# Performance work log

Measured on AMD Instinct MI355X. Metric: run time of the kernel, lower is better.

Reference implementation:

```python
import jax, jax.numpy as jnp
import numpy as np

N = 500000      # nodes
F_IN = 10       # node_features
HID = 32        # DCRNN hidden
OUT = 2         # out_features
E = 8000000     # edges (unused in math since K=1, kept for interface fidelity)


def setup_inputs() -> dict:
    key = jax.random.key(0)
    ks = jax.random.split(key, 12)
    d_in = F_IN + HID  # 42: DConv input is cat([X, H])
    s = 0.1
    return {
        "x": jax.random.normal(ks[0], (N, F_IN), dtype=jnp.float32),
        "edge_index": jax.random.randint(ks[1], (2, E), 0, N, dtype=jnp.int64),
        "edge_weight": jax.random.uniform(ks[2], (E,), dtype=jnp.float32),
        "h": jax.random.normal(ks[3], (N, HID), dtype=jnp.float32),
        # DConv weights: torch shape (2, K=1, in, out); K dim squeezed -> (2, in, out)
        "W_z": jax.random.normal(ks[4], (2, d_in, HID), dtype=jnp.float32) * s,
        "b_z": jnp.zeros((HID,), dtype=jnp.float32),
        "W_r": jax.random.normal(ks[5], (2, d_in, HID), dtype=jnp.float32) * s,
        "b_r": jnp.zeros((HID,), dtype=jnp.float32),
        "W_h": jax.random.normal(ks[6], (2, d_in, HID), dtype=jnp.float32) * s,
        "b_h": jnp.zeros((HID,), dtype=jnp.float32),
        "W_lin": jax.random.normal(ks[7], (OUT, HID), dtype=jnp.float32) * s,
        "b_lin": jnp.zeros((OUT,), dtype=jnp.float32),
    }


def _dconv_k1(xh, W, b):
    # K=1 DConv: out/in diffusion weights collapse to a single dense transform
    return xh @ (W[0] + W[1]) + b


def reference(x, edge_index, edge_weight, h, W_z, b_z, W_r, b_r, W_h, b_h, W_lin, b_lin):
    # DCRNN GRU step (edge_index/edge_weight unused because K=1)
    xh = jnp.concatenate([x, h], axis=1)                  # [N, F_IN+HID]
    z = jax.nn.sigmoid(_dconv_k1(xh, W_z, b_z))           # update gate
    r = jax.nn.sigmoid(_dconv_k1(xh, W_r, b_r))           # reset gate
    xrh = jnp.concatenate([x, r * h], axis=1)
    h_tilde = jnp.tanh(_dconv_k1(xrh, W_h, b_h))
    h_new = z * h + (1.0 - z) * h_tilde                   # [N, HID]
    out = jnp.maximum(h_new, 0.0) @ W_lin.T + b_lin       # ReLU + Linear head, [N, OUT]
    return (out, h_new)
```

## Files before the change

### kernel.cpp

```cpp
#include <hip/hip_runtime.h>
#include <stdint.h>

static constexpr int N_NODES = 500000;
static constexpr int STR     = 56;

typedef __attribute__((ext_vector_type(8))) short short8;
typedef __attribute__((ext_vector_type(4))) float f32x4;


__device__ __forceinline__ float bfdec(uint32_t b){
  union{uint32_t u; float f;} c; c.u = b << 16; return c.f;
}
__device__ __forceinline__ uint32_t bfrne(float f){
  union{float f; uint32_t u;} c; c.f = f;
  return (c.u + 0x7fffu + ((c.u >> 16) & 1u)) >> 16;
}
__device__ __forceinline__ uint32_t pack2(float a, float b){
  return bfrne(a) | (bfrne(b) << 16);
}
__device__ __forceinline__ float sigmoid_fast(float x){
  float e = __expf(-x);
  return __builtin_amdgcn_rcpf(1.0f + e);
}
__device__ __forceinline__ float tanh_fast(float x){
  float e = __expf(2.0f * x);
  return 1.0f - 2.0f * __builtin_amdgcn_rcpf(e + 1.0f);
}

__device__ bool detect_f32_words(const uint32_t* w, int K){
  float m = 0.0f;
  for (int i = 0; i < K; i++) m = fmaxf(m, fabsf(bfdec(w[i] & 0xffffu)));
  return !(m < 1e6f);
}
__device__ __forceinline__ float wload(const void* p, int idx, bool f32w){
  if (f32w) return ((const float*)p)[idx];
  return bfdec(((const uint16_t*)p)[idx]);
}

__global__ void prep_kernel(const void* __restrict__ Wz,
                            const void* __restrict__ bz,
                            const void* __restrict__ Wr,
                            const void* __restrict__ br,
                            const void* __restrict__ Wh,
                            const void* __restrict__ bh,
                            const void* __restrict__ Wl,
                            const void* __restrict__ bl,
                            const uint32_t* __restrict__ xg,
                            const uint32_t* __restrict__ hg,
                            float* __restrict__ ws)
{
  const bool f32w = detect_f32_words((const uint32_t*)Wz, 64);
  uint16_t* wsh = (uint16_t*)ws;
  float*    wsf = ws;
  int i = blockIdx.x * 256 + threadIdx.x;
  if (i < 5376) {
    float v = 0.0f;
    if (i < 3584) {
      int col = i / STR, k = i - col * STR;
      if (k < 42) {
        const void* Wp = (col < 32) ? Wz : Wr;
        int j = (col < 32) ? col : col - 32;
        int src = k * 32 + j;
        v = wload(Wp, src, f32w) + wload(Wp, 1344 + src, f32w);
      }
    } else {
      int t2 = i - 3584;
      int col = t2 / STR, k = t2 - col * STR;
      if (k < 42) {
        int src = k * 32 + col;
        v = wload(Wh, src, f32w) + wload(Wh, 1344 + src, f32w);
      }
    }
    wsh[i] = (uint16_t)bfrne(v);
  } else if (i < 5440) {
    int r = i - 5376;
    wsh[i] = (uint16_t)bfrne(wload(Wl, r, f32w));
  } else if (i < 5538) {
    int r = i - 5440;
    if      (r < 32) wsf[2720 + r]      = wload(bz, r,     f32w);
    else if (r < 64) wsf[2752 + (r-32)] = wload(br, r-32,  f32w);
    else if (r < 96) wsf[2784 + (r-64)] = wload(bh, r-64,  f32w);
    else             wsf[2816 + (r-96)] = wload(bl, r-96,  f32w);
  } else if (i == 5568) {
    wsf[2818] = detect_f32_words(xg, 256) ? 1.0f : 0.0f;
  } else if (i == 5569) {
    wsf[2819] = detect_f32_words(hg, 256) ? 1.0f : 0.0f;
  }
}

__global__ __launch_bounds__(256, 4) void dcrnn_kernel(
    const uint32_t* __restrict__ xg,
    const uint32_t* __restrict__ hg,
    const float*    __restrict__ ws,
    float* __restrict__ out0,
    float* __restrict__ outh)
{
  __shared__ __align__(16) uint16_t w_u16[96 * STR];
  __shared__ __align__(16) uint16_t xh_u16[256 * STR];

  const int t  = threadIdx.x;
  const int nd = blockIdx.x * 256 + t;
  const bool valid = nd < N_NODES;
  const float* wsf = ws;
  const bool x_f32 = wsf[2818] != 0.0f;
  const bool h_f32 = wsf[2819] != 0.0f;

  const uint4* wsq = (const uint4*)ws;
  for (int i = t; i < 672; i += 256) ((uint4*)w_u16)[i] = wsq[i];

  uint32_t rw[24];
  #pragma unroll
  for (int i = 0; i < 24; i++) rw[i] = 0u;
  if (valid) {
    if (x_f32) {
      const float2* xr = (const float2*)((const float*)xg + (size_t)nd * 10);
      #pragma unroll
      for (int i = 0; i < 5; i++){ float2 v = xr[i]; rw[i] = pack2(v.x, v.y); }
    } else {
      const uint32_t* xr = xg + (size_t)nd * 5;
      #pragma unroll
      for (int i = 0; i < 5; i++) rw[i] = xr[i];
    }
    if (h_f32) {
      const float4* hr = (const float4*)((const float*)hg + (size_t)nd * 32);
      #pragma unroll
      for (int i = 0; i < 8; i++){
        float4 v = hr[i];
        rw[5 + 2*i]     = pack2(v.x, v.y);
        rw[5 + 2*i + 1] = pack2(v.z, v.w);
      }
    } else {
      const uint4* hr = (const uint4*)(hg + (size_t)nd * 16);
      #pragma unroll
      for (int i = 0; i < 4; i++){
        uint4 v = hr[i];
        rw[5 + 4*i]     = v.x; rw[5 + 4*i + 1] = v.y;
        rw[5 + 4*i + 2] = v.z; rw[5 + 4*i + 3] = v.w;
      }
    }
  }
  {
    uint4* dst = (uint4*)(xh_u16 + t * STR);
    #pragma unroll
    for (int c = 0; c < 6; c++)
      dst[c] = make_uint4(rw[4*c], rw[4*c+1], rw[4*c+2], rw[4*c+3]);
  }
  __syncthreads();

  const int l = t & 63, w = t >> 6;
  const int lo16 = l & 15, g = l >> 4;
  uint16_t* xwm = xh_u16 + (w * 64) * STR;

  const float bzc0 = wsf[2720 + lo16], bzc1 = wsf[2736 + lo16];
  const float brc0 = wsf[2752 + lo16], brc1 = wsf[2768 + lo16];
  const float bhc0 = wsf[2784 + lo16], bhc1 = wsf[2800 + lo16];
  const float blc  = (lo16 < 2) ? wsf[2816 + lo16] : 0.0f;

  const short8 zero8 = {0,0,0,0,0,0,0,0};

  short8 bzr_lo[4], bzr_hi[4];
  #pragma unroll
  for (int nt = 0; nt < 4; nt++){
    const uint16_t* brow = w_u16 + (nt*16 + lo16) * STR;
    bzr_lo[nt] = *(const short8*)(brow + g*8);
    bzr_hi[nt] = zero8;
    if (g < 2) bzr_hi[nt] = *(const short8*)(brow + 32 + g*8);
  }
  short8 bh_lo[2], bh_hi[2];
  #pragma unroll
  for (int nt = 0; nt < 2; nt++){
    const uint16_t* brow = w_u16 + 3584 + (nt*16 + lo16) * STR;
    bh_lo[nt] = *(const short8*)(brow + g*8);
    bh_hi[nt] = zero8;
    if (g < 2) bh_hi[nt] = *(const short8*)(brow + 32 + g*8);
  }
  short8 bO = zero8;
  if (lo16 < 2) bO = *(const short8*)((const uint16_t*)ws + 5376 + lo16*32 + g*8);

  #pragma unroll
  for (int mt = 0; mt < 4; mt++){
    const uint16_t* arow = xwm + (mt*16 + lo16) * STR;
    short8 a0 = *(const short8*)(arow + g*8);
    short8 a1 = zero8;
    if (g < 2) a1 = *(const short8*)(arow + 32 + g*8);

    f32x4 accZ0 = {bzc0,bzc0,bzc0,bzc0};
    f32x4 accZ1 = {bzc1,bzc1,bzc1,bzc1};
    f32x4 accR0 = {brc0,brc0,brc0,brc0};
    f32x4 accR1 = {brc1,brc1,brc1,brc1};
    accZ0 = __builtin_amdgcn_mfma_f32_16x16x32_bf16(a0, bzr_lo[0], accZ0, 0,0,0);
    accZ0 = __builtin_amdgcn_mfma_f32_16x16x32_bf16(a1, bzr_hi[0], accZ0, 0,0,0);
    accZ1 = __builtin_amdgcn_mfma_f32_16x16x32_bf16(a0, bzr_lo[1], accZ1, 0,0,0);
    accZ1 = __builtin_amdgcn_mfma_f32_16x16x32_bf16(a1, bzr_hi[1], accZ1, 0,0,0);
    accR0 = __builtin_amdgcn_mfma_f32_16x16x32_bf16(a0, bzr_lo[2], accR0, 0,0,0);
    accR0 = __builtin_amdgcn_mfma_f32_16x16x32_bf16(a1, bzr_hi[2], accR0, 0,0,0);
    accR1 = __builtin_amdgcn_mfma_f32_16x16x32_bf16(a0, bzr_lo[3], accR1, 0,0,0);
    accR1 = __builtin_amdgcn_mfma_f32_16x16x32_bf16(a1, bzr_hi[3], accR1, 0,0,0);

    f32x4 hs0, hs1;
    #pragma unroll
    for (int q = 0; q < 4; q++){
      int row = mt*16 + g*4 + q;
      uint16_t* p0 = xwm + row*STR + 10 + lo16;
      uint16_t* p1 = xwm + row*STR + 26 + lo16;
      float h0 = bfdec(*p0), h1 = bfdec(*p1);
      float r0 = sigmoid_fast(accR0[q]);
      float r1 = sigmoid_fast(accR1[q]);
      *p0 = (uint16_t)bfrne(r0 * h0);
      *p1 = (uint16_t)bfrne(r1 * h1);
      hs0[q] = h0; hs1[q] = h1;
    }
    asm volatile("s_waitcnt lgkmcnt(0)" ::: "memory");

    f32x4 accH0 = {bhc0,bhc0,bhc0,bhc0};
    f32x4 accH1 = {bhc1,bhc1,bhc1,bhc1};
    short8 c0 = *(const short8*)(arow + g*8);
    short8 c1 = zero8;
    if (g < 2) c1 = *(const short8*)(arow + 32 + g*8);
    accH0 = __builtin_amdgcn_mfma_f32_16x16x32_bf16(c0, bh_lo[0], accH0, 0,0,0);
    accH0 = __builtin_amdgcn_mfma_f32_16x16x32_bf16(c1, bh_hi[0], accH0, 0,0,0);
    accH1 = __builtin_amdgcn_mfma_f32_16x16x32_bf16(c0, bh_lo[1], accH1, 0,0,0);
    accH1 = __builtin_amdgcn_mfma_f32_16x16x32_bf16(c1, bh_hi[1], accH1, 0,0,0);

    #pragma unroll
    for (int q = 0; q < 4; q++){
      int row  = mt*16 + g*4 + q;
      int node = blockIdx.x*256 + w*64 + row;
      float z0 = sigmoid_fast(accZ0[q]);
      float z1 = sigmoid_fast(accZ1[q]);
      float t0 = tanh_fast(accH0[q]);
      float t1 = tanh_fast(accH1[q]);
      float hn0 = fmaf(z0, hs0[q] - t0, t0);
      float hn1 = fmaf(z1, hs1[q] - t1, t1);
      if (node < N_NODES){
        outh[(size_t)node*32 + lo16]      = hn0;
        outh[(size_t)node*32 + 16 + lo16] = hn1;
      }
      *(xwm + row*STR + lo16)      = (uint16_t)bfrne(fmaxf(hn0, 0.0f));
      *(xwm + row*STR + 16 + lo16) = (uint16_t)bfrne(fmaxf(hn1, 0.0f));
    }
    asm volatile("s_waitcnt lgkmcnt(0)" ::: "memory");

    short8 aO = *(const short8*)(arow + g*8);
    f32x4 accO = {blc, blc, blc, blc};
    accO = __builtin_amdgcn_mfma_f32_16x16x32_bf16(aO, bO, accO, 0,0,0);
    #pragma unroll
    for (int q = 0; q < 4; q++){
      int node = blockIdx.x*256 + w*64 + mt*16 + g*4 + q;
      if (lo16 < 2 && node < N_NODES)
        out0[(size_t)node*2 + lo16] = accO[q];
    }
  }
}

extern "C" void kernel_launch(void* const* d_in, const int* in_sizes, int n_in,
                              void* d_out, int out_size, void* d_ws, size_t ws_size,
                              hipStream_t stream) {
  const uint32_t* x = (const uint32_t*)d_in[0];
  const uint32_t* h = (const uint32_t*)d_in[3];

  float* ws = (float*)d_ws;

  prep_kernel<<<22, 256, 0, stream>>>(d_in[4], d_in[5], d_in[6], d_in[7],
                                      d_in[8], d_in[9], d_in[10], d_in[11],
                                      x, h, ws);

  float* outf = (float*)d_out;
  float* out0 = outf;
  float* outh = outf + (size_t)2 * N_NODES;
  dcrnn_kernel<<<(N_NODES + 255) / 256, 256, 0, stream>>>(
      x, h, ws, out0, outh);
}
```

Before: 248.6 us.

## Load weights directly from global, shrink blocks, compute output head per-thread

Drops the shared-memory staging of the weight matrices and has each lane read its MFMA B fragments straight from the workspace in global memory (cached). Block size shrinks from 256 to 128 threads with half the LDS, which should allow more resident blocks per CU. The final Linear head moves from a sparse MFMA with per-lane strided stores to a per-thread FMA dot product over the bf16 ReLU'd hidden state, written as one float2 per node. Costs are more global/L2 traffic for the weights, more scalar FMAs, and a workspace layout change. There is also a possible LDS hazard: the per-thread read at the end covers rows written by other lanes of the same wave without a barrier.

Measured after the change: 243.5 us. -2.1%, faster.

```diff
diff --git a/kernel.cpp b/kernel.cpp
--- a/kernel.cpp
+++ b/kernel.cpp
@@ -11,6 +11,8 @@
 __device__ __forceinline__ float bfdec(uint32_t b){
   union{uint32_t u; float f;} c; c.u = b << 16; return c.f;
 }
+__device__ __forceinline__ float bf_lo(uint32_t u){ union{uint32_t u; float f;} c; c.u = u << 16; return c.f; }
+__device__ __forceinline__ float bf_hi(uint32_t u){ union{uint32_t u; float f;} c; c.u = u & 0xffff0000u; return c.f; }
 __device__ __forceinline__ uint32_t bfrne(float f){
   union{float f; uint32_t u;} c; c.f = f;
   return (c.u + 0x7fffu + ((c.u >> 16) & 1u)) >> 16;
@@ -72,41 +74,36 @@
       }
     }
     wsh[i] = (uint16_t)bfrne(v);
-  } else if (i < 5440) {
+  } else if (i < 5538) {
     int r = i - 5376;
-    wsh[i] = (uint16_t)bfrne(wload(Wl, r, f32w));
-  } else if (i < 5538) {
-    int r = i - 5440;
-    if      (r < 32) wsf[2720 + r]      = wload(bz, r,     f32w);
-    else if (r < 64) wsf[2752 + (r-32)] = wload(br, r-32,  f32w);
-    else if (r < 96) wsf[2784 + (r-64)] = wload(bh, r-64,  f32w);
-    else             wsf[2816 + (r-96)] = wload(bl, r-96,  f32w);
+    if      (r < 32)  wsf[2688 + r]       = wload(bz, r,     f32w);
+    else if (r < 64)  wsf[2720 + (r-32)]  = wload(br, r-32,  f32w);
+    else if (r < 96)  wsf[2752 + (r-64)]  = wload(bh, r-64,  f32w);
+    else if (r < 160) wsf[2784 + (r-96)]  = wload(Wl, r-96,  f32w);
+    else              wsf[2848 + (r-160)] = wload(bl, r-160, f32w);
   } else if (i == 5568) {
-    wsf[2818] = detect_f32_words(xg, 256) ? 1.0f : 0.0f;
+    wsf[2850] = detect_f32_words(xg, 256) ? 1.0f : 0.0f;
   } else if (i == 5569) {
-    wsf[2819] = detect_f32_words(hg, 256) ? 1.0f : 0.0f;
-  }
-}
-
-__global__ __launch_bounds__(256, 4) void dcrnn_kernel(
+    wsf[2851] = detect_f32_words(hg, 256) ? 1.0f : 0.0f;
+  }
+}
+
+__global__ __launch_bounds__(128, 4) void dcrnn_kernel(
     const uint32_t* __restrict__ xg,
     const uint32_t* __restrict__ hg,
     const float*    __restrict__ ws,
     float* __restrict__ out0,
     float* __restrict__ outh)
 {
-  __shared__ __align__(16) uint16_t w_u16[96 * STR];
-  __shared__ __align__(16) uint16_t xh_u16[256 * STR];
+  __shared__ __align__(16) uint16_t xh_u16[128 * STR];
 
   const int t  = threadIdx.x;
-  const int nd = blockIdx.x * 256 + t;
+  const int nd = blockIdx.x * 128 + t;
   const bool valid = nd < N_NODES;
   const float* wsf = ws;
-  const bool x_f32 = wsf[2818] != 0.0f;
-  const bool h_f32 = wsf[2819] != 0.0f;
-
-  const uint4* wsq = (const uint4*)ws;
-  for (int i = t; i < 672; i += 256) ((uint4*)w_u16)[i] = wsq[i];
+  const uint16_t* wsh = (const uint16_t*)ws;
+  const bool x_f32 = wsf[2850] != 0.0f;
+  const bool h_f32 = wsf[2851] != 0.0f;
 
   uint32_t rw[24];
   #pragma unroll
@@ -145,37 +142,35 @@
     for (int c = 0; c < 6; c++)
       dst[c] = make_uint4(rw[4*c], rw[4*c+1], rw[4*c+2], rw[4*c+3]);
   }
-  __syncthreads();
 
   const int l = t & 63, w = t >> 6;
   const int lo16 = l & 15, g = l >> 4;
-  uint16_t* xwm = xh_u16 + (w * 64) * STR;
-
-  const float bzc0 = wsf[2720 + lo16], bzc1 = wsf[2736 + lo16];
-  const float brc0 = wsf[2752 + lo16], brc1 = wsf[2768 + lo16];
-  const float bhc0 = wsf[2784 + lo16], bhc1 = wsf[2800 + lo16];
-  const float blc  = (lo16 < 2) ? wsf[2816 + lo16] : 0.0f;
-
   const short8 zero8 = {0,0,0,0,0,0,0,0};
 
   short8 bzr_lo[4], bzr_hi[4];
   #pragma unroll
   for (int nt = 0; nt < 4; nt++){
-    const uint16_t* brow = w_u16 + (nt*16 + lo16) * STR;
+    const uint16_t* brow = wsh + (nt*16 + lo16) * STR;
     bzr_lo[nt] = *(const short8*)(brow + g*8);
     bzr_hi[nt] = zero8;
     if (g < 2) bzr_hi[nt] = *(const short8*)(brow + 32 + g*8);
   }
-  short8 bh_lo[2], bh_hi[2];
+  short8 bhf_lo[2], bhf_hi[2];
   #pragma unroll
   for (int nt = 0; nt < 2; nt++){
-    const uint16_t* brow = w_u16 + 3584 + (nt*16 + lo16) * STR;
-    bh_lo[nt] = *(const short8*)(brow + g*8);
-    bh_hi[nt] = zero8;
-    if (g < 2) bh_hi[nt] = *(const short8*)(brow + 32 + g*8);
-  }
-  short8 bO = zero8;
-  if (lo16 < 2) bO = *(const short8*)((const uint16_t*)ws + 5376 + lo16*32 + g*8);
+    const uint16_t* brow = wsh + 3584 + (nt*16 + lo16) * STR;
+    bhf_lo[nt] = *(const short8*)(brow + g*8);
+    bhf_hi[nt] = zero8;
+    if (g < 2) bhf_hi[nt] = *(const short8*)(brow + 32 + g*8);
+  }
+
+  const float bzc0 = wsf[2688 + lo16], bzc1 = wsf[2704 + lo16];
+  const float brc0 = wsf[2720 + lo16], brc1 = wsf[2736 + lo16];
+  const float bhc0 = wsf[2752 + lo16], bhc1 = wsf[2768 + lo16];
+
+  __syncthreads();
+
+  uint16_t* xwm = xh_u16 + (w * 64) * STR;
 
   #pragma unroll
   for (int mt = 0; mt < 4; mt++){
@@ -217,15 +212,15 @@
     short8 c0 = *(const short8*)(arow + g*8);
     short8 c1 = zero8;
     if (g < 2) c1 = *(const short8*)(arow + 32 + g*8);
-    accH0 = __builtin_amdgcn_mfma_f32_16x16x32_bf16(c0, bh_lo[0], accH0, 0,0,0);
-    accH0 = __builtin_amdgcn_mfma_f32_16x16x32_bf16(c1, bh_hi[0], accH0, 0,0,0);
-    accH1 = __builtin_amdgcn_mfma_f32_16x16x32_bf16(c0, bh_lo[1], accH1, 0,0,0);
-    accH1 = __builtin_amdgcn_mfma_f32_16x16x32_bf16(c1, bh_hi[1], accH1, 0,0,0);
+    accH0 = __builtin_amdgcn_mfma_f32_16x16x32_bf16(c0, bhf_lo[0], accH0, 0,0,0);
+    accH0 = __builtin_amdgcn_mfma_f32_16x16x32_bf16(c1, bhf_hi[0], accH0, 0,0,0);
+    accH1 = __builtin_amdgcn_mfma_f32_16x16x32_bf16(c0, bhf_lo[1], accH1, 0,0,0);
+    accH1 = __builtin_amdgcn_mfma_f32_16x16x32_bf16(c1, bhf_hi[1], accH1, 0,0,0);
 
     #pragma unroll
     for (int q = 0; q < 4; q++){
       int row  = mt*16 + g*4 + q;
-      int node = blockIdx.x*256 + w*64 + row;
+      int node = blockIdx.x*128 + w*64 + row;
       float z0 = sigmoid_fast(accZ0[q]);
       float z1 = sigmoid_fast(accZ1[q]);
       float t0 = tanh_fast(accH0[q]);
@@ -239,17 +234,28 @@
       *(xwm + row*STR + lo16)      = (uint16_t)bfrne(fmaxf(hn0, 0.0f));
       *(xwm + row*STR + 16 + lo16) = (uint16_t)bfrne(fmaxf(hn1, 0.0f));
     }
-    asm volatile("s_waitcnt lgkmcnt(0)" ::: "memory");
-
-    short8 aO = *(const short8*)(arow + g*8);
-    f32x4 accO = {blc, blc, blc, blc};
-    accO = __builtin_amdgcn_mfma_f32_16x16x32_bf16(aO, bO, accO, 0,0,0);
-    #pragma unroll
-    for (int q = 0; q < 4; q++){
-      int node = blockIdx.x*256 + w*64 + mt*16 + g*4 + q;
-      if (lo16 < 2 && node < N_NODES)
-        out0[(size_t)node*2 + lo16] = accO[q];
-    }
+  }
+
+  asm volatile("s_waitcnt lgkmcnt(0)" ::: "memory");
+  if (valid){
+    float o0 = wsf[2848], o1 = wsf[2849];
+    const uint4* hq = (const uint4*)(xh_u16 + t * STR);
+    #pragma unroll
+    for (int i = 0; i < 4; i++){
+      uint4 v = hq[i];
+      uint32_t wv[4] = {v.x, v.y, v.z, v.w};
+      #pragma unroll
+      for (int j = 0; j < 4; j++){
+        int c = i*8 + j*2;
+        float v0 = bf_lo(wv[j]);
+        float v1 = bf_hi(wv[j]);
+        o0 = fmaf(v0, wsf[2784 + c],     o0);
+        o1 = fmaf(v0, wsf[2816 + c],     o1);
+        o0 = fmaf(v1, wsf[2784 + c + 1], o0);
+        o1 = fmaf(v1, wsf[2816 + c + 1], o1);
+      }
+    }
+    ((float2*)out0)[nd] = make_float2(o0, o1);
   }
 }
 
@@ -268,6 +274,6 @@
   float* outf = (float*)d_out;
   float* out0 = outf;
   float* outh = outf + (size_t)2 * N_NODES;
-  dcrnn_kernel<<<(N_NODES + 255) / 256, 256, 0, stream>>>(
+  dcrnn_kernel<<<(N_NODES + 127) / 128, 128, 0, stream>>>(
       x, h, ws, out0, outh);
 }
```
